# Performance work log

Measured on AMD Instinct MI355X. Metric: run time of the kernel, lower is better.

## Reference

```python
import jax, jax.numpy as jnp
import numpy as np

I = 512
H = 512
B = 64
T = 512

def _lstm_step(W_ih, W_hh, b_ih, b_hh):
    def step(carry, xt):
        h, c = carry
        # gates in torch LSTMCell order: i, f, g, o
        gates = xt @ W_ih.T + b_ih + h @ W_hh.T + b_hh  # [B, 4H]
        i, f, g, o = jnp.split(gates, 4, axis=-1)
        c = jax.nn.sigmoid(f) * c + jax.nn.sigmoid(i) * jnp.tanh(g)
        h = jax.nn.sigmoid(o) * jnp.tanh(c)
        return (h, c), h
    return step

def setup_inputs() -> dict:
    key = jax.random.key(0)
    ks = jax.random.split(key, 9)
    s = 1.0 / np.sqrt(H)  # torch LSTMCell init: U(-1/sqrt(H), 1/sqrt(H))
    u = lambda k, shp: jax.random.uniform(k, shp, jnp.float32, -s, s)
    return {
        "xs": jax.random.normal(ks[0], (B, T, I), jnp.float32),
        "W_ih_f": u(ks[1], (4 * H, I)), "W_hh_f": u(ks[2], (4 * H, H)),
        "b_ih_f": u(ks[3], (4 * H,)), "b_hh_f": u(ks[4], (4 * H,)),
        "W_ih_b": u(ks[5], (4 * H, I)), "W_hh_b": u(ks[6], (4 * H, H)),
        "b_ih_b": u(ks[7], (4 * H,)), "b_hh_b": u(ks[8], (4 * H,)),
    }

def reference(xs, W_ih_f, W_hh_f, b_ih_f, b_hh_f, W_ih_b, W_hh_b, b_ih_b, b_hh_b):
    x = jnp.transpose(xs, (1, 0, 2))  # batch_first -> [T, B, I]
    b, h = x.shape[1], W_hh_f.shape[1]
    init = (jnp.zeros((b, h), x.dtype), jnp.zeros((b, h), x.dtype))
    _, hs_fwd = jax.lax.scan(_lstm_step(W_ih_f, W_hh_f, b_ih_f, b_hh_f), init, x)
    # reverse direction: scan backward, outputs land at original time indices
    _, hs_bwd = jax.lax.scan(_lstm_step(W_ih_b, W_hh_b, b_ih_b, b_hh_b), init, x, reverse=True)
    rst = jnp.concatenate([hs_fwd, hs_bwd], axis=-1)  # [T, B, 2H]
    return jnp.transpose(rst, (1, 0, 2))  # back to [B, T, 2H]
```

## Files before the change

### kernel.cpp

```cpp
#include <hip/hip_runtime.h>
#include <math.h>

#define B 64
#define T 512
#define II 512
#define H 512
#define NBLK 256

typedef float f32x4 __attribute__((ext_vector_type(4)));
typedef short s16x8 __attribute__((ext_vector_type(8)));
typedef unsigned long long u64;

__device__ __forceinline__ unsigned short f2b(float f){
  union { float f; unsigned u; } v; v.f = f;
  unsigned r = v.u + 0x7fffu + ((v.u >> 16) & 1u);
  return (unsigned short)(r >> 16);
}

__global__ void init_ws(unsigned* p, int n){
  int i = blockIdx.x*blockDim.x + threadIdx.x;
  for (; i < n; i += gridDim.x*blockDim.x) p[i] = 0u;
}

__global__ __launch_bounds__(256, 1) void lstm_persistent(
    const float* __restrict__ xs,
    const float* __restrict__ Wih_f, const float* __restrict__ Whh_f,
    const float* __restrict__ bih_f, const float* __restrict__ bhh_f,
    const float* __restrict__ Wih_b, const float* __restrict__ Whh_b,
    const float* __restrict__ bih_b, const float* __restrict__ bhh_b,
    float* __restrict__ out,
    unsigned* __restrict__ flags,
    unsigned short* __restrict__ hbuf0, unsigned short* __restrict__ hbuf1)
{
  __shared__ unsigned short Wlds[4*16*1024];
  __shared__ unsigned short Hlds[16*512];
  __shared__ float g_lds[4][16][16];
  __shared__ float bias_s[64];

  const int tid = threadIdx.x;
  const int bx = blockIdx.x;
  const int dir   = bx >> 7;
  const int qtile = bx & 31;
  const int btile = (bx >> 5) & 3;
  const int q0 = qtile * 16;
  const int b0 = btile * 16;

  const float* __restrict__ Wih = dir ? Wih_b : Wih_f;
  const float* __restrict__ Whh = dir ? Whh_b : Whh_f;
  const float* __restrict__ bih = dir ? bih_b : bih_f;
  const float* __restrict__ bhh = dir ? bhh_b : bhh_f;

  for (int it = 0; it < 32; ++it){
    int idx = it * 256 + tid;
    int c64 = idx >> 7;
    int k   = (idx & 127) * 8;
    int cg  = (c64 >> 4) * H + q0 + (c64 & 15);
    const float* src = (k < II) ? (Wih + (size_t)cg * II + k)
                                : (Whh + (size_t)cg * H + (k - II));
    float4 lo = *(const float4*)src;
    float4 hi = *(const float4*)(src + 4);
    s16x8 v;
    v[0]=(short)f2b(lo.x); v[1]=(short)f2b(lo.y); v[2]=(short)f2b(lo.z); v[3]=(short)f2b(lo.w);
    v[4]=(short)f2b(hi.x); v[5]=(short)f2b(hi.y); v[6]=(short)f2b(hi.z); v[7]=(short)f2b(hi.w);
    unsigned byte = ((unsigned)c64 * 2048u + (unsigned)k * 2u) ^ (((unsigned)(c64 & 7)) << 4);
    *(s16x8*)((char*)Wlds + byte) = v;
  }
  if (tid < 64){
    int g = tid >> 4, jj = tid & 15;
    int cg = g * H + q0 + jj;
    bias_s[tid] = bih[cg] + bhh[cg];
  }
  __syncthreads();

  const int w = tid >> 6;
  const int l = tid & 63;
  const int arow = b0 + (l & 15);
  const int kgrp = (l >> 4) * 8;
  const int c64w = (w << 4) | (l & 15);
  const unsigned swz = ((unsigned)(c64w & 7)) << 4;
  const unsigned wbase = (unsigned)c64w * 2048u;
  const unsigned hrowb = ((unsigned)(l & 15)) * 1024u;
  const unsigned hswz  = ((unsigned)(l & 7)) << 4;

  const int eb = tid >> 4;
  const int ej = tid & 15;
  const int hr = tid >> 4;
  const int hc = (tid & 15) * 32;
  float c_reg = 0.f;

  const size_t hbase = (size_t)dir * B * H;
  const unsigned gflag0 = (unsigned)(bx & ~31);
  const unsigned myflag = (unsigned)bx << 5;

  s16x8 a_x[16];
  {
    const int t0 = dir ? (T-1) : 0;
    const float* xrow = xs + ((size_t)arow * T + t0) * II + kgrp;
    #pragma unroll
    for (int ks = 0; ks < 16; ++ks){
      float4 lo = *(const float4*)(xrow + ks*32);
      float4 hi = *(const float4*)(xrow + ks*32 + 4);
      s16x8 a;
      a[0]=(short)f2b(lo.x); a[1]=(short)f2b(lo.y); a[2]=(short)f2b(lo.z); a[3]=(short)f2b(lo.w);
      a[4]=(short)f2b(hi.x); a[5]=(short)f2b(hi.y); a[6]=(short)f2b(hi.z); a[7]=(short)f2b(hi.w);
      a_x[ks] = a;
    }
  }

  #pragma unroll 1
  for (int s = 0; s < T; ++s){
    const int t = dir ? (T - 1 - s) : s;
    const unsigned short* __restrict__ hin  = (s & 1) ? hbuf1 : hbuf0;
    unsigned short* __restrict__       hout = (s & 1) ? hbuf0 : hbuf1;

    u64 hv[8];
    {
      const u64* hsrc = (const u64*)(hin + hbase + (size_t)(b0 + hr) * H + hc);
      #pragma unroll
      for (int i = 0; i < 8; ++i)
        hv[i] = __hip_atomic_load(hsrc + i, __ATOMIC_RELAXED, __HIP_MEMORY_SCOPE_AGENT);
    }

    f32x4 acc0 = {0.f,0.f,0.f,0.f}, acc1 = {0.f,0.f,0.f,0.f};
    #pragma unroll
    for (int ks = 0; ks < 16; ++ks){
      unsigned byte = (wbase + (unsigned)(ks*32 + kgrp) * 2u) ^ swz;
      s16x8 bfr = *(const s16x8*)((const char*)Wlds + byte);
      acc0 = __builtin_amdgcn_mfma_f32_16x16x32_bf16(a_x[ks], bfr, acc0, 0, 0, 0);
    }

    #pragma unroll
    for (int i = 0; i < 8; ++i){
      unsigned byte = ((unsigned)hr * 1024u + (unsigned)(hc + i*4) * 2u)
                    ^ (((unsigned)(hr & 7)) << 4);
      *(u64*)((char*)Hlds + byte) = hv[i];
    }
    __syncthreads();

    #pragma unroll
    for (int ks = 0; ks < 16; ++ks){
      unsigned hbyte = (hrowb + (unsigned)(ks*32 + kgrp) * 2u) ^ hswz;
      s16x8 a = *(const s16x8*)((const char*)Hlds + hbyte);
      unsigned byte = (wbase + (unsigned)(II + ks*32 + kgrp) * 2u) ^ swz;
      s16x8 bfr = *(const s16x8*)((const char*)Wlds + byte);
      acc1 = __builtin_amdgcn_mfma_f32_16x16x32_bf16(a, bfr, acc1, 0, 0, 0);
    }

    #pragma unroll
    for (int r = 0; r < 4; ++r){
      int bl = (l >> 4) * 4 + r;
      g_lds[w][bl][l & 15] = acc0[r] + acc1[r];
    }
    __syncthreads();

    float hn;
    {
      float gi = g_lds[0][eb][ej] + bias_s[ej];
      float gf = g_lds[1][eb][ej] + bias_s[16 + ej];
      float gg = g_lds[2][eb][ej] + bias_s[32 + ej];
      float go = g_lds[3][eb][ej] + bias_s[48 + ej];
      float si = 1.f/(1.f + __expf(-gi));
      float sf = 1.f/(1.f + __expf(-gf));
      float tg = tanhf(gg);
      float so = 1.f/(1.f + __expf(-go));
      c_reg = sf * c_reg + si * tg;
      hn = so * tanhf(c_reg);
      unsigned hb = (unsigned)f2b(hn);
      unsigned pv = (unsigned)__shfl_xor((int)hb, 1, 64);
      if (!(tid & 1)){
        unsigned idx = (unsigned)((hbase + (size_t)(b0 + eb) * H + (q0 + ej)) >> 1);
        __hip_atomic_store((unsigned*)hout + idx, hb | (pv << 16),
                           __ATOMIC_RELAXED, __HIP_MEMORY_SCOPE_AGENT);
      }
    }

    __syncthreads();
    if (s + 1 < T && tid == 0)
      __hip_atomic_store(&flags[myflag], (unsigned)(s+1),
                         __ATOMIC_RELAXED, __HIP_MEMORY_SCOPE_AGENT);

    out[((size_t)(b0+eb) * T + t) * (2*H) + (size_t)dir * H + (q0 + ej)] = hn;
    if (s + 1 < T){
      const int tn = dir ? (T - 2 - s) : (s + 1);
      const float* xrow = xs + ((size_t)arow * T + tn) * II + kgrp;
      #pragma unroll
      for (int ks = 0; ks < 16; ++ks){
        float4 lo = *(const float4*)(xrow + ks*32);
        float4 hi = *(const float4*)(xrow + ks*32 + 4);
        s16x8 a;
        a[0]=(short)f2b(lo.x); a[1]=(short)f2b(lo.y); a[2]=(short)f2b(lo.z); a[3]=(short)f2b(lo.w);
        a[4]=(short)f2b(hi.x); a[5]=(short)f2b(hi.y); a[6]=(short)f2b(hi.z); a[7]=(short)f2b(hi.w);
        a_x[ks] = a;
      }

      for (;;){
        int done = 1;
        if (tid < 32)
          done = (__hip_atomic_load(&flags[(gflag0 + (unsigned)tid) << 5],
                                    __ATOMIC_RELAXED, __HIP_MEMORY_SCOPE_AGENT)
                  > (unsigned)s);
        if (__syncthreads_and(done)) break;
        __builtin_amdgcn_s_sleep(1);
      }
    }
  }
}

extern "C" void kernel_launch(void* const* d_in, const int* in_sizes, int n_in,
                              void* d_out, int out_size, void* d_ws, size_t ws_size,
                              hipStream_t stream)
{
  const float* xs    = (const float*)d_in[0];
  const float* Wih_f = (const float*)d_in[1];
  const float* Whh_f = (const float*)d_in[2];
  const float* bih_f = (const float*)d_in[3];
  const float* bhh_f = (const float*)d_in[4];
  const float* Wih_b = (const float*)d_in[5];
  const float* Whh_b = (const float*)d_in[6];
  const float* bih_b = (const float*)d_in[7];
  const float* bhh_b = (const float*)d_in[8];
  float* out = (float*)d_out;

  char* ws = (char*)d_ws;
  unsigned* flags = (unsigned*)ws;
  unsigned short* hbuf0 = (unsigned short*)(ws + 32768);
  unsigned short* hbuf1 = (unsigned short*)(ws + 32768 + 2*B*H*2);

  const int init_u32 = (32768 + 2*(2*B*H*2)) / 4;
  init_ws<<<128, 256, 0, stream>>>((unsigned*)ws, init_u32);

  lstm_persistent<<<NBLK, 256, 0, stream>>>(
      xs, Wih_f, Whh_f, bih_f, bhh_f,
      Wih_b, Whh_b, bih_b, bhh_b,
      out, flags, hbuf0, hbuf1);
}
```

Baseline: 3.177 ms.

## Replace flag barrier with step-tagged hidden-state words and split MFMA chains

Drops the per-block flag array and the cross-block spin barrier. Each hidden value is now stored as a 32-bit word holding the bf16 value and the step counter, so consumers poll their own h slice until every tag matches the current step. This removes one global round trip and a block-wide syncthreads per timestep. It also splits each MFMA accumulation into two independent chains, uses packed bf16 convert instructions, and uses fast rcp-based sigmoid and tanh. The trade-off is twice the hidden-state traffic per read and polling that needs no global fence.

```diff
diff --git a/kernel.cpp b/kernel.cpp
--- a/kernel.cpp
+++ b/kernel.cpp
@@ -9,15 +9,37 @@
 
 typedef float f32x4 __attribute__((ext_vector_type(4)));
 typedef short s16x8 __attribute__((ext_vector_type(8)));
+typedef unsigned u32;
 typedef unsigned long long u64;
 
+union pk8 { s16x8 v; u32 u[4]; };
+union pk4 { uint4 q; u32 u[4]; };
+
 __device__ __forceinline__ unsigned short f2b(float f){
-  union { float f; unsigned u; } v; v.f = f;
-  unsigned r = v.u + 0x7fffu + ((v.u >> 16) & 1u);
+  union { float f; u32 u; } v; v.f = f;
+  u32 r = v.u + 0x7fffu + ((v.u >> 16) & 1u);
   return (unsigned short)(r >> 16);
 }
 
-__global__ void init_ws(unsigned* p, int n){
+__device__ __forceinline__ s16x8 cvt8(float4 lo, float4 hi){
+  pk8 r;
+  asm("v_cvt_pk_bf16_f32 %0, %1, %2" : "=v"(r.u[0]) : "v"(lo.x), "v"(lo.y));
+  asm("v_cvt_pk_bf16_f32 %0, %1, %2" : "=v"(r.u[1]) : "v"(lo.z), "v"(lo.w));
+  asm("v_cvt_pk_bf16_f32 %0, %1, %2" : "=v"(r.u[2]) : "v"(hi.x), "v"(hi.y));
+  asm("v_cvt_pk_bf16_f32 %0, %1, %2" : "=v"(r.u[3]) : "v"(hi.z), "v"(hi.w));
+  return r.v;
+}
+
+__device__ __forceinline__ float sigm_(float x){
+  return __builtin_amdgcn_rcpf(1.f + __expf(-x));
+}
+__device__ __forceinline__ float tanh_(float x){
+  float t = __expf(-2.f * fabsf(x));
+  float r = (1.f - t) * __builtin_amdgcn_rcpf(1.f + t);
+  return copysignf(r, x);
+}
+
+__global__ void init_ws(u32* p, int n){
   int i = blockIdx.x*blockDim.x + threadIdx.x;
   for (; i < n; i += gridDim.x*blockDim.x) p[i] = 0u;
 }
@@ -29,8 +51,7 @@
     const float* __restrict__ Wih_b, const float* __restrict__ Whh_b,
     const float* __restrict__ bih_b, const float* __restrict__ bhh_b,
     float* __restrict__ out,
-    unsigned* __restrict__ flags,
-    unsigned short* __restrict__ hbuf0, unsigned short* __restrict__ hbuf1)
+    u32* __restrict__ hbuf0, u32* __restrict__ hbuf1)
 {
   __shared__ unsigned short Wlds[4*16*1024];
   __shared__ unsigned short Hlds[16*512];
@@ -62,7 +83,7 @@
     s16x8 v;
     v[0]=(short)f2b(lo.x); v[1]=(short)f2b(lo.y); v[2]=(short)f2b(lo.z); v[3]=(short)f2b(lo.w);
     v[4]=(short)f2b(hi.x); v[5]=(short)f2b(hi.y); v[6]=(short)f2b(hi.z); v[7]=(short)f2b(hi.w);
-    unsigned byte = ((unsigned)c64 * 2048u + (unsigned)k * 2u) ^ (((unsigned)(c64 & 7)) << 4);
+    u32 byte = ((u32)c64 * 2048u + (u32)k * 2u) ^ (((u32)(c64 & 7)) << 4);
     *(s16x8*)((char*)Wlds + byte) = v;
   }
   if (tid < 64){
@@ -77,131 +98,135 @@
   const int arow = b0 + (l & 15);
   const int kgrp = (l >> 4) * 8;
   const int c64w = (w << 4) | (l & 15);
-  const unsigned swz = ((unsigned)(c64w & 7)) << 4;
-  const unsigned wbase = (unsigned)c64w * 2048u;
-  const unsigned hrowb = ((unsigned)(l & 15)) * 1024u;
-  const unsigned hswz  = ((unsigned)(l & 7)) << 4;
+  const u32 swz   = ((u32)(c64w & 7)) << 4;
+  const u32 wbase = (u32)c64w * 2048u;
+  const u32 hrowb = ((u32)(l & 15)) * 1024u;
+  const u32 hswz  = ((u32)(l & 7)) << 4;
+
+  const int hr   = tid & 15;
+  const int hcg  = tid >> 4;
+  const u32 hwbyte = (u32)hr * 1024u + (u32)hcg * 64u;
+  const u32 hwswz  = ((u32)(hr & 7)) << 4;
 
   const int eb = tid >> 4;
   const int ej = tid & 15;
-  const int hr = tid >> 4;
-  const int hc = (tid & 15) * 32;
   float c_reg = 0.f;
 
   const size_t hbase = (size_t)dir * B * H;
-  const unsigned gflag0 = (unsigned)(bx & ~31);
-  const unsigned myflag = (unsigned)bx << 5;
+  const size_t hoff  = hbase + (size_t)(b0 + hr) * H + (size_t)hcg * 32;
 
   s16x8 a_x[16];
   {
     const int t0 = dir ? (T-1) : 0;
     const float* xrow = xs + ((size_t)arow * T + t0) * II + kgrp;
     #pragma unroll
-    for (int ks = 0; ks < 16; ++ks){
-      float4 lo = *(const float4*)(xrow + ks*32);
-      float4 hi = *(const float4*)(xrow + ks*32 + 4);
-      s16x8 a;
-      a[0]=(short)f2b(lo.x); a[1]=(short)f2b(lo.y); a[2]=(short)f2b(lo.z); a[3]=(short)f2b(lo.w);
-      a[4]=(short)f2b(hi.x); a[5]=(short)f2b(hi.y); a[6]=(short)f2b(hi.z); a[7]=(short)f2b(hi.w);
-      a_x[ks] = a;
-    }
+    for (int ks = 0; ks < 16; ++ks)
+      a_x[ks] = cvt8(*(const float4*)(xrow + ks*32), *(const float4*)(xrow + ks*32 + 4));
   }
 
   #pragma unroll 1
   for (int s = 0; s < T; ++s){
     const int t = dir ? (T - 1 - s) : s;
-    const unsigned short* __restrict__ hin  = (s & 1) ? hbuf1 : hbuf0;
-    unsigned short* __restrict__       hout = (s & 1) ? hbuf0 : hbuf1;
-
-    u64 hv[8];
-    {
-      const u64* hsrc = (const u64*)(hin + hbase + (size_t)(b0 + hr) * H + hc);
+    const u32* __restrict__ hin  = (s & 1) ? hbuf1 : hbuf0;
+    u32* __restrict__       hout = (s & 1) ? hbuf0 : hbuf1;
+
+    u64 hv[16];
+    {
+      const u64* hsrc = (const u64*)(hin + hoff);
       #pragma unroll
-      for (int i = 0; i < 8; ++i)
+      for (int i = 0; i < 16; ++i)
         hv[i] = __hip_atomic_load(hsrc + i, __ATOMIC_RELAXED, __HIP_MEMORY_SCOPE_AGENT);
     }
 
-    f32x4 acc0 = {0.f,0.f,0.f,0.f}, acc1 = {0.f,0.f,0.f,0.f};
-    #pragma unroll
-    for (int ks = 0; ks < 16; ++ks){
-      unsigned byte = (wbase + (unsigned)(ks*32 + kgrp) * 2u) ^ swz;
-      s16x8 bfr = *(const s16x8*)((const char*)Wlds + byte);
-      acc0 = __builtin_amdgcn_mfma_f32_16x16x32_bf16(a_x[ks], bfr, acc0, 0, 0, 0);
-    }
-
-    #pragma unroll
-    for (int i = 0; i < 8; ++i){
-      unsigned byte = ((unsigned)hr * 1024u + (unsigned)(hc + i*4) * 2u)
-                    ^ (((unsigned)(hr & 7)) << 4);
-      *(u64*)((char*)Hlds + byte) = hv[i];
+    f32x4 acc_xa = {0.f,0.f,0.f,0.f}, acc_xb = {0.f,0.f,0.f,0.f};
+    #pragma unroll
+    for (int ks = 0; ks < 8; ++ks){
+      u32 byte0 = (wbase + (u32)(ks*32 + kgrp) * 2u) ^ swz;
+      u32 byte1 = (wbase + (u32)((ks+8)*32 + kgrp) * 2u) ^ swz;
+      s16x8 b0f = *(const s16x8*)((const char*)Wlds + byte0);
+      s16x8 b1f = *(const s16x8*)((const char*)Wlds + byte1);
+      acc_xa = __builtin_amdgcn_mfma_f32_16x16x32_bf16(a_x[ks],   b0f, acc_xa, 0, 0, 0);
+      acc_xb = __builtin_amdgcn_mfma_f32_16x16x32_bf16(a_x[ks+8], b1f, acc_xb, 0, 0, 0);
+    }
+
+    {
+      const u64 expect = ((u64)(u32)s) | (((u64)(u32)s) << 32);
+      const u64 tmask  = 0x0000FFFF0000FFFFull;
+      for (;;){
+        u64 diff = 0;
+        #pragma unroll
+        for (int i = 0; i < 16; ++i) diff |= (hv[i] ^ expect) & tmask;
+        if (diff == 0) break;
+        __builtin_amdgcn_s_sleep(1);
+        const u64* hsrc = (const u64*)(hin + hoff);
+        #pragma unroll
+        for (int i = 0; i < 16; ++i)
+          hv[i] = __hip_atomic_load(hsrc + i, __ATOMIC_RELAXED, __HIP_MEMORY_SCOPE_AGENT);
+      }
+    }
+
+    {
+      #pragma unroll
+      for (int i = 0; i < 4; ++i){
+        pk4 p;
+        #pragma unroll
+        for (int j = 0; j < 4; ++j){
+          u32 w0 = (u32)hv[i*4+j];
+          u32 w1 = (u32)(hv[i*4+j] >> 32);
+          p.u[j] = (w0 >> 16) | (w1 & 0xffff0000u);
+        }
+        u32 byte = (hwbyte + (u32)i * 16u) ^ hwswz;
+        *(uint4*)((char*)Hlds + byte) = p.q;
+      }
     }
     __syncthreads();
 
-    #pragma unroll
-    for (int ks = 0; ks < 16; ++ks){
-      unsigned hbyte = (hrowb + (unsigned)(ks*32 + kgrp) * 2u) ^ hswz;
-      s16x8 a = *(const s16x8*)((const char*)Hlds + hbyte);
-      unsigned byte = (wbase + (unsigned)(II + ks*32 + kgrp) * 2u) ^ swz;
-      s16x8 bfr = *(const s16x8*)((const char*)Wlds + byte);
-      acc1 = __builtin_amdgcn_mfma_f32_16x16x32_bf16(a, bfr, acc1, 0, 0, 0);
+    f32x4 acc_ha = {0.f,0.f,0.f,0.f}, acc_hb = {0.f,0.f,0.f,0.f};
+    #pragma unroll
+    for (int ks = 0; ks < 8; ++ks){
+      u32 hb0 = (hrowb + (u32)(ks*32 + kgrp) * 2u) ^ hswz;
+      u32 hb1 = (hrowb + (u32)((ks+8)*32 + kgrp) * 2u) ^ hswz;
+      s16x8 a0 = *(const s16x8*)((const char*)Hlds + hb0);
+      s16x8 a1 = *(const s16x8*)((const char*)Hlds + hb1);
+      u32 byte0 = (wbase + (u32)(II + ks*32 + kgrp) * 2u) ^ swz;
+      u32 byte1 = (wbase + (u32)(II + (ks+8)*32 + kgrp) * 2u) ^ swz;
+      s16x8 b0f = *(const s16x8*)((const char*)Wlds + byte0);
+      s16x8 b1f = *(const s16x8*)((const char*)Wlds + byte1);
+      acc_ha = __builtin_amdgcn_mfma_f32_16x16x32_bf16(a0, b0f, acc_ha, 0, 0, 0);
+      acc_hb = __builtin_amdgcn_mfma_f32_16x16x32_bf16(a1, b1f, acc_hb, 0, 0, 0);
     }
 
     #pragma unroll
     for (int r = 0; r < 4; ++r){
       int bl = (l >> 4) * 4 + r;
-      g_lds[w][bl][l & 15] = acc0[r] + acc1[r];
+      g_lds[w][bl][l & 15] = acc_xa[r] + acc_xb[r] + acc_ha[r] + acc_hb[r];
     }
     __syncthreads();
 
-    float hn;
     {
       float gi = g_lds[0][eb][ej] + bias_s[ej];
       float gf = g_lds[1][eb][ej] + bias_s[16 + ej];
       float gg = g_lds[2][eb][ej] + bias_s[32 + ej];
       float go = g_lds[3][eb][ej] + bias_s[48 + ej];
-      float si = 1.f/(1.f + __expf(-gi));
-      float sf = 1.f/(1.f + __expf(-gf));
-      float tg = tanhf(gg);
-      float so = 1.f/(1.f + __expf(-go));
+      float si = sigm_(gi);
+      float sf = sigm_(gf);
+      float tg = tanh_(gg);
+      float so = sigm_(go);
       c_reg = sf * c_reg + si * tg;
-      hn = so * tanhf(c_reg);
-      unsigned hb = (unsigned)f2b(hn);
-      unsigned pv = (unsigned)__shfl_xor((int)hb, 1, 64);
-      if (!(tid & 1)){
-        unsigned idx = (unsigned)((hbase + (size_t)(b0 + eb) * H + (q0 + ej)) >> 1);
-        __hip_atomic_store((unsigned*)hout + idx, hb | (pv << 16),
-                           __ATOMIC_RELAXED, __HIP_MEMORY_SCOPE_AGENT);
-      }
-    }
-
-    __syncthreads();
-    if (s + 1 < T && tid == 0)
-      __hip_atomic_store(&flags[myflag], (unsigned)(s+1),
+      float hn = so * tanh_(c_reg);
+      u32 hb = (u32)f2b(hn);
+      size_t idx = hbase + (size_t)(b0 + eb) * H + (size_t)(q0 + ej);
+      __hip_atomic_store(hout + idx, (hb << 16) | (u32)(s + 1),
                          __ATOMIC_RELAXED, __HIP_MEMORY_SCOPE_AGENT);
-
-    out[((size_t)(b0+eb) * T + t) * (2*H) + (size_t)dir * H + (q0 + ej)] = hn;
+      out[((size_t)(b0+eb) * T + t) * (2*H) + (size_t)dir * H + (q0 + ej)] = hn;
+    }
+
     if (s + 1 < T){
       const int tn = dir ? (T - 2 - s) : (s + 1);
       const float* xrow = xs + ((size_t)arow * T + tn) * II + kgrp;
       #pragma unroll
-      for (int ks = 0; ks < 16; ++ks){
-        float4 lo = *(const float4*)(xrow + ks*32);
-        float4 hi = *(const float4*)(xrow + ks*32 + 4);
-        s16x8 a;
-        a[0]=(short)f2b(lo.x); a[1]=(short)f2b(lo.y); a[2]=(short)f2b(lo.z); a[3]=(short)f2b(lo.w);
-        a[4]=(short)f2b(hi.x); a[5]=(short)f2b(hi.y); a[6]=(short)f2b(hi.z); a[7]=(short)f2b(hi.w);
-        a_x[ks] = a;
-      }
-
-      for (;;){
-        int done = 1;
-        if (tid < 32)
-          done = (__hip_atomic_load(&flags[(gflag0 + (unsigned)tid) << 5],
-                                    __ATOMIC_RELAXED, __HIP_MEMORY_SCOPE_AGENT)
-                  > (unsigned)s);
-        if (__syncthreads_and(done)) break;
-        __builtin_amdgcn_s_sleep(1);
-      }
+      for (int ks = 0; ks < 16; ++ks)
+        a_x[ks] = cvt8(*(const float4*)(xrow + ks*32), *(const float4*)(xrow + ks*32 + 4));
     }
   }
 }
@@ -222,15 +247,13 @@
   float* out = (float*)d_out;
 
   char* ws = (char*)d_ws;
-  unsigned* flags = (unsigned*)ws;
-  unsigned short* hbuf0 = (unsigned short*)(ws + 32768);
-  unsigned short* hbuf1 = (unsigned short*)(ws + 32768 + 2*B*H*2);
-
-  const int init_u32 = (32768 + 2*(2*B*H*2)) / 4;
-  init_ws<<<128, 256, 0, stream>>>((unsigned*)ws, init_u32);
+  u32* hbuf0 = (u32*)ws;
+  u32* hbuf1 = (u32*)(ws + 2*B*H*4);
+
+  init_ws<<<128, 256, 0, stream>>>((u32*)ws, 2*(2*B*H));
 
   lstm_persistent<<<NBLK, 256, 0, stream>>>(
       xs, Wih_f, Whh_f, bih_f, bhh_f,
       Wih_b, Whh_b, bih_b, bhh_b,
-      out, flags, hbuf0, hbuf1);
-}
+      out, hbuf0, hbuf1);
+}
```

After: 3.857 ms. 1.21x slower.
